# Kernel optimization log

Hardware: AMD Instinct MI355X
Metric: run time of the kernel (lower is better)

Reference implementation:

```python
import jax, jax.numpy as jnp
import numpy as np

SCALE = 0.1  # module's p / self.scale

def setup_inputs() -> dict:
    key = jax.random.key(0)
    k1, k2, k3 = jax.random.split(key, 3)
    d = 2048
    x = jax.random.normal(k1, (8192, d), dtype=jnp.float32)
    # torch Linear: weight [out, in], y = x @ W.T + b
    W = jax.random.normal(k2, (d, d), dtype=jnp.float32) * (1.0 / np.sqrt(d))
    b = jax.random.normal(k3, (d,), dtype=jnp.float32) * (1.0 / np.sqrt(d))
    return {"x": x, "W": W, "b": b}

def reference(x, W, b):
    # y = Linear(x); z = y * scale; return z.sum(-1)
    y = jnp.einsum('bi,oi->bo', x, W) + b  # [B, d]
    return (y * SCALE).sum(axis=-1)        # [B]
```

## Files before the change

### kernel.cpp

```cpp
#include <hip/hip_runtime.h>

#define DIM   2048
#define NROW  8192
#define SCALE 0.1f


__global__ __launch_bounds__(256) void init_kernel(const float* __restrict__ b,
                                                   float* __restrict__ ws) {
    const int t = threadIdx.x;
    for (int i = t; i < DIM; i += 256) ws[i] = 0.0f;

    float s = 0.0f;
#pragma unroll
    for (int k = 0; k < DIM / 256; ++k) s += b[k * 256 + t];

#pragma unroll
    for (int off = 32; off > 0; off >>= 1) s += __shfl_down(s, off, 64);

    __shared__ float part[4];
    const int lane = t & 63, wave = t >> 6;
    if (lane == 0) part[wave] = s;
    __syncthreads();
    if (t == 0) ws[DIM] = part[0] + part[1] + part[2] + part[3];
}

#define ROWS_PER_BLK 32
__global__ __launch_bounds__(256) void colsum_kernel(const float* __restrict__ W,
                                                     float* __restrict__ ws) {
    const int col4 = blockIdx.x * 256 + threadIdx.x;
    const int row0 = blockIdx.y * ROWS_PER_BLK;
    const float4* __restrict__ W4 = (const float4*)W;

    float ax = 0.f, ay = 0.f, az = 0.f, aw = 0.f;
#pragma unroll 8
    for (int r = 0; r < ROWS_PER_BLK; ++r) {
        float4 v = W4[(size_t)(row0 + r) * (DIM / 4) + col4];
        ax += v.x; ay += v.y; az += v.z; aw += v.w;
    }
    float* dst = ws + col4 * 4;
    atomicAdd(dst + 0, ax);
    atomicAdd(dst + 1, ay);
    atomicAdd(dst + 2, az);
    atomicAdd(dst + 3, aw);
}

__global__ __launch_bounds__(256) void rowdot_kernel(const float* __restrict__ x,
                                                     const float* __restrict__ ws,
                                                     float* __restrict__ out) {
    const int row = blockIdx.x;
    const int t = threadIdx.x;
    const float4* __restrict__ xr = (const float4*)(x + (size_t)row * DIM);
    const float4* __restrict__ wc = (const float4*)ws;

    float s = 0.0f;
#pragma unroll
    for (int k = 0; k < DIM / 4 / 256; ++k) {
        float4 xv = xr[k * 256 + t];
        float4 wv = wc[k * 256 + t];
        s += xv.x * wv.x + xv.y * wv.y + xv.z * wv.z + xv.w * wv.w;
    }

#pragma unroll
    for (int off = 32; off > 0; off >>= 1) s += __shfl_down(s, off, 64);

    __shared__ float part[4];
    const int lane = t & 63, wave = t >> 6;
    if (lane == 0) part[wave] = s;
    __syncthreads();
    if (t == 0) {
        float tot = part[0] + part[1] + part[2] + part[3];
        out[row] = SCALE * (tot + ws[DIM]);
    }
}

extern "C" void kernel_launch(void* const* d_in, const int* in_sizes, int n_in,
                              void* d_out, int out_size, void* d_ws, size_t ws_size,
                              hipStream_t stream) {
    const float* x = (const float*)d_in[0];
    const float* W = (const float*)d_in[1];
    const float* b = (const float*)d_in[2];
    float* out = (float*)d_out;
    float* ws  = (float*)d_ws;

    init_kernel<<<1, 256, 0, stream>>>(b, ws);

    dim3 cgrid(DIM / 1024, DIM / ROWS_PER_BLK);
    colsum_kernel<<<cgrid, 256, 0, stream>>>(W, ws);

    rowdot_kernel<<<NROW, 256, 0, stream>>>(x, ws, out);
}
```

Baseline: 110.4 us.

## Fold bias sum into colsum kernel, memset workspace, one wave per row

Drops the separate init kernel: the workspace is zeroed with hipMemsetAsync and the bias sum is computed by an extra block appended to the column-sum kernel. The column-sum grid changes to 256 blocks of 16 rows each, with the loop fully unrolled. The row-dot kernel now gives each 64-lane wave its own row, which removes the LDS reduction and __syncthreads, and launches a quarter as many blocks. The goal is to cut launch and synchronisation overhead around the memory-bound pass over x. In exchange there are twice as many atomics on the column sums, and the memset is still a separate operation on the stream.

```diff
diff --git a/kernel.cpp b/kernel.cpp
--- a/kernel.cpp
+++ b/kernel.cpp
@@ -5,35 +5,32 @@
 #define SCALE 0.1f
 
 
-__global__ __launch_bounds__(256) void init_kernel(const float* __restrict__ b,
-                                                   float* __restrict__ ws) {
+__global__ __launch_bounds__(256) void colsum_kernel(const float* __restrict__ W,
+                                                     const float* __restrict__ b,
+                                                     float* __restrict__ ws) {
+    const int blk = blockIdx.x;
     const int t = threadIdx.x;
-    for (int i = t; i < DIM; i += 256) ws[i] = 0.0f;
 
-    float s = 0.0f;
+    if (blk == 256) {
+        float s = 0.0f;
 #pragma unroll
-    for (int k = 0; k < DIM / 256; ++k) s += b[k * 256 + t];
+        for (int k = 0; k < DIM / 256; ++k) s += b[k * 256 + t];
+#pragma unroll
+        for (int off = 32; off > 0; off >>= 1) s += __shfl_down(s, off, 64);
+        __shared__ float part[4];
+        if ((t & 63) == 0) part[t >> 6] = s;
+        __syncthreads();
+        if (t == 0) ws[DIM] = part[0] + part[1] + part[2] + part[3];
+        return;
+    }
 
-#pragma unroll
-    for (int off = 32; off > 0; off >>= 1) s += __shfl_down(s, off, 64);
-
-    __shared__ float part[4];
-    const int lane = t & 63, wave = t >> 6;
-    if (lane == 0) part[wave] = s;
-    __syncthreads();
-    if (t == 0) ws[DIM] = part[0] + part[1] + part[2] + part[3];
-}
-
-#define ROWS_PER_BLK 32
-__global__ __launch_bounds__(256) void colsum_kernel(const float* __restrict__ W,
-                                                     float* __restrict__ ws) {
-    const int col4 = blockIdx.x * 256 + threadIdx.x;
-    const int row0 = blockIdx.y * ROWS_PER_BLK;
+    const int col4 = (blk & 1) * 256 + t;
+    const int row0 = (blk >> 1) * 16;
     const float4* __restrict__ W4 = (const float4*)W;
 
     float ax = 0.f, ay = 0.f, az = 0.f, aw = 0.f;
-#pragma unroll 8
-    for (int r = 0; r < ROWS_PER_BLK; ++r) {
+#pragma unroll
+    for (int r = 0; r < 16; ++r) {
         float4 v = W4[(size_t)(row0 + r) * (DIM / 4) + col4];
         ax += v.x; ay += v.y; az += v.z; aw += v.w;
     }
@@ -47,30 +44,24 @@
 __global__ __launch_bounds__(256) void rowdot_kernel(const float* __restrict__ x,
                                                      const float* __restrict__ ws,
                                                      float* __restrict__ out) {
-    const int row = blockIdx.x;
-    const int t = threadIdx.x;
-    const float4* __restrict__ xr = (const float4*)(x + (size_t)row * DIM);
+    const int row  = (int)((blockIdx.x * 256u + threadIdx.x) >> 6);
+    const int lane = threadIdx.x & 63;
+    const float bsum = ws[DIM];
+
+    const float4* __restrict__ xr = (const float4*)x + (size_t)row * (DIM / 4);
     const float4* __restrict__ wc = (const float4*)ws;
 
     float s = 0.0f;
 #pragma unroll
-    for (int k = 0; k < DIM / 4 / 256; ++k) {
-        float4 xv = xr[k * 256 + t];
-        float4 wv = wc[k * 256 + t];
+    for (int j = 0; j < 8; ++j) {
+        float4 xv = xr[j * 64 + lane];
+        float4 wv = wc[j * 64 + lane];
         s += xv.x * wv.x + xv.y * wv.y + xv.z * wv.z + xv.w * wv.w;
     }
-
 #pragma unroll
     for (int off = 32; off > 0; off >>= 1) s += __shfl_down(s, off, 64);
 
-    __shared__ float part[4];
-    const int lane = t & 63, wave = t >> 6;
-    if (lane == 0) part[wave] = s;
-    __syncthreads();
-    if (t == 0) {
-        float tot = part[0] + part[1] + part[2] + part[3];
-        out[row] = SCALE * (tot + ws[DIM]);
-    }
+    if (lane == 0) out[row] = SCALE * (s + bsum);
 }
 
 extern "C" void kernel_launch(void* const* d_in, const int* in_sizes, int n_in,
@@ -82,10 +73,8 @@
     float* out = (float*)d_out;
     float* ws  = (float*)d_ws;
 
-    init_kernel<<<1, 256, 0, stream>>>(b, ws);
+    hipMemsetAsync(ws, 0, (DIM + 1) * sizeof(float), stream);
 
-    dim3 cgrid(DIM / 1024, DIM / ROWS_PER_BLK);
-    colsum_kernel<<<cgrid, 256, 0, stream>>>(W, ws);
-
-    rowdot_kernel<<<NROW, 256, 0, stream>>>(x, ws, out);
+    colsum_kernel<<<257, 256, 0, stream>>>(W, b, ws);
+    rowdot_kernel<<<NROW / 4, 256, 0, stream>>>(x, ws, out);
 }
```

Measured after the change: 120.8 us. 9.5% more time.
